# Optimization experiments

Hardware: AMD Instinct MI355X
Metric: run time of the kernel (lower is better)

## Reference

```python
import jax, jax.numpy as jnp
import numpy as np

S = 4      # num_residual_streams
V = 1      # num_input_views
ITERS = 20 # sinkhorn iters
B = 2      # batch
N = 4096   # seq len
D = 2048   # dim (num_fracs=1 so dim_eff == dim)


def setup_inputs() -> dict:
    key = jax.random.key(0)
    ks = jax.random.split(key, 6)
    return dict(
        residuals=jax.random.normal(ks[0], (B * S, N, D), jnp.float32),
        gamma=0.1 * jax.random.normal(ks[1], (S * D,), jnp.float32),
        dyn_alpha_fn=0.02 * jax.random.normal(ks[2], (S * D, S * (S + V)), jnp.float32),
        static_alpha=jax.random.normal(ks[3], (S, S + V), jnp.float32),
        pre_branch_scale=0.01 * jnp.ones((1,), jnp.float32),
        residual_scale=0.01 * jnp.ones((1,), jnp.float32),
        dyn_beta_fn=0.02 * jax.random.normal(ks[4], (S * D, S), jnp.float32),
        static_beta=jax.random.normal(ks[5], (S,), jnp.float32),
        h_post_scale=jnp.float32(0.01),
    )


def _sinkhorn(log_a, iters):
    # alternating row/col normalization in log space over last two axes
    def body(_, la):
        la = la - jax.scipy.special.logsumexp(la, axis=-2, keepdims=True)
        return la - jax.scipy.special.logsumexp(la, axis=-1, keepdims=True)
    return jnp.exp(jax.lax.fori_loop(0, iters, body, log_a))


def reference(residuals, gamma, dyn_alpha_fn, static_alpha, pre_branch_scale,
              residual_scale, dyn_beta_fn, static_beta, h_post_scale):
    bs, n, d = residuals.shape
    b = bs // S
    # '(b s) n d -> b n s d'
    r = residuals.reshape(b, S, n, d).transpose(0, 2, 1, 3)  # [b,n,S,d]
    flat = r.reshape(b, n, S * d)
    # RMSNorm: F.normalize(x, dim=-1) * sqrt(S*d) * (gamma + 1)
    nrm = flat / jnp.maximum(jnp.linalg.norm(flat, axis=-1, keepdims=True), 1e-12)
    normed = nrm * jnp.sqrt(jnp.float32(S * d)) * (gamma + 1.0)  # [b,n,S*d]

    wc = (normed @ dyn_alpha_fn).reshape(b, n, S, S + V)  # dynamic gate weights
    alpha_scale = jnp.concatenate([
        jnp.broadcast_to(pre_branch_scale, (V,)),
        jnp.broadcast_to(residual_scale, (S,)),
    ])  # [S+V]
    alpha = wc * alpha_scale + static_alpha  # [b,n,S,S+V]
    alpha_pre = jax.nn.sigmoid(alpha[..., :V])            # [b,n,S,V]
    alpha_res = _sinkhorn(alpha[..., V:], ITERS)          # doubly-stochastic [b,n,S,S]
    alpha_full = jnp.concatenate([alpha_pre, alpha_res], axis=-1)  # [b,n,S,1+S]

    # mix streams: '... s t, ... s d -> ... t d'
    mix = jnp.einsum('bnst,bnsd->bntd', alpha_full, r)  # [b,n,1+S,d]
    branch_input = mix[..., 0, :]       # [b,n,d]
    res_mix = mix[..., 1:, :]           # [b,n,S,d]

    beta = jax.nn.sigmoid((normed @ dyn_beta_fn) * h_post_scale + static_beta) * 2.0  # [b,n,S]

    # branch = identity -> branch_output == branch_input
    # depth connection: 'b n d, b n s -> b n s d', then add residual streams
    out = branch_input[..., None, :] * beta[..., :, None] + res_mix  # [b,n,S,d]
    # 'b n s d -> (b s) n d'
    return out.transpose(0, 2, 1, 3).reshape(b * S, n, d)
```

## Files before the change

### kernel.cpp

```cpp
#include <hip/hip_runtime.h>
#include <hip/hip_bf16.h>

typedef float f32x4 __attribute__((ext_vector_type(4)));
typedef float f32x16 __attribute__((ext_vector_type(16)));
typedef unsigned int u32;
typedef u32 u32x2 __attribute__((ext_vector_type(2)));
typedef u32 u32x4 __attribute__((ext_vector_type(4)));
typedef short bf16x8 __attribute__((ext_vector_type(8)));

#define SD 8192
#define NROWS 8192
#define NN 4096
#define DD 2048
#define DTP 4104

__device__ __forceinline__ u32 bfr(float f) {
    u32 u = __float_as_uint(f);
    return (u + 0x7fffu + ((u >> 16) & 1u)) >> 16;
}
__device__ __forceinline__ float blo(u32 u) { return __uint_as_float(u << 16); }
__device__ __forceinline__ float bhi(u32 u) { return __uint_as_float(u & 0xffff0000u); }

__global__ void k0_prep(const float* __restrict__ gamma,
                        const float* __restrict__ daf,
                        const float* __restrict__ dbf,
                        unsigned short* __restrict__ Wfrag) {
    int idx = blockIdx.x * 256 + threadIdx.x;
    if (idx >= 32 * SD) return;
    const int e    = idx & 7;
    const int lane = (idx >> 3) & 63;
    const int st   = (idx >> 9) & 63;
    const int wv   = idx >> 15;
    const int outk = lane & 31;
    const int j    = wv * 1024 + st * 16 + ((lane >> 5) & 1) * 8 + e;
    unsigned short v = 0;
    if (outk < 24) {
        float g = gamma[j] + 1.0f;
        float w = (outk < 20) ? daf[j * 20 + outk] : dbf[j * 4 + (outk - 20)];
        v = (unsigned short)bfr(w * g);
    }
    Wfrag[idx] = v;
}

__global__ __launch_bounds__(512) void kf(const float* __restrict__ res,
                                          const unsigned short* __restrict__ Wfrag,
                                          const float* __restrict__ sa,
                                          const float* __restrict__ sb,
                                          const float* __restrict__ pbs,
                                          const float* __restrict__ rsc,
                                          const float* __restrict__ hps,
                                          float* __restrict__ out) {
    __shared__ u32 dTp[4][DTP];
    __shared__ float pc[8][4][32];
    __shared__ float red[4][32];
    __shared__ float ssqw[8];
    __shared__ float coefS[4][16];

    const int tid  = threadIdx.x;
    const int wv   = tid >> 6;
    const int lane = tid & 63;
    const int row0 = blockIdx.x * 4;
    const int b    = row0 >> 12;
    const int n0   = row0 & (NN - 1);
    const int r    = tid >> 7;
    const int rem  = tid & 127;

    const float* rowbase = res + ((size_t)(b * 4) * NN + (n0 + r)) * DD;
    f32x4 ssq4 = {0.f, 0.f, 0.f, 0.f};
#pragma unroll 1
    for (int h = 0; h < 4; ++h) {
        f32x4 v[4];
#pragma unroll
        for (int i = 0; i < 4; ++i) {
            const int q  = h * 4 + i;
            const int j0 = (rem + 128 * q) * 4;
            const int s  = j0 >> 11, d = j0 & 2047;
            v[i] = __builtin_nontemporal_load((const f32x4*)(rowbase + (size_t)s * NN * DD + d));
        }
#pragma unroll
        for (int i = 0; i < 4; ++i) {
            ssq4 += v[i] * v[i];
            u32 lo, hi;
            asm("v_cvt_pk_bf16_f32 %0, %1, %2" : "=v"(lo) : "v"(v[i].x), "v"(v[i].y));
            asm("v_cvt_pk_bf16_f32 %0, %1, %2" : "=v"(hi) : "v"(v[i].z), "v"(v[i].w));
            const int jp = (rem + 128 * (h * 4 + i)) * 2;
            *(u32x2*)&dTp[r][jp] = (u32x2){lo, hi};
        }
    }
    float ssq = ssq4.x + ssq4.y + ssq4.z + ssq4.w;
    ssq += __shfl_xor(ssq, 1);  ssq += __shfl_xor(ssq, 2);
    ssq += __shfl_xor(ssq, 4);  ssq += __shfl_xor(ssq, 8);
    ssq += __shfl_xor(ssq, 16); ssq += __shfl_xor(ssq, 32);
    if (lane == 0) ssqw[wv] = ssq;
    __syncthreads();

    {
        f32x16 acc;
#pragma unroll
        for (int i = 0; i < 16; ++i) acc[i] = 0.f;
        const u32* abase = &dTp[lane & 3][wv * 512 + (lane >> 5) * 4];
        const unsigned short* wbase = Wfrag + ((size_t)wv * 64 * 64 + lane) * 8;
#pragma unroll 1
        for (int g = 0; g < 8; ++g) {
            u32x4 bu[8];
#pragma unroll
            for (int s = 0; s < 8; ++s)
                bu[s] = *(const u32x4*)(wbase + (size_t)(g * 8 + s) * 64 * 8);
#pragma unroll
            for (int s = 0; s < 8; ++s) {
                const u32x4 au = *(const u32x4*)(abase + (g * 8 + s) * 8);
                acc = __builtin_amdgcn_mfma_f32_32x32x16_bf16(
                    __builtin_bit_cast(bf16x8, au), __builtin_bit_cast(bf16x8, bu[s]), acc, 0, 0, 0);
            }
        }
        if (lane < 32) {
#pragma unroll
            for (int gg = 0; gg < 4; ++gg) pc[wv][gg][lane] = acc[gg];
        }
    }
    __syncthreads();
    if (tid < 128) {
        const int rr = tid >> 5, c = tid & 31;
        float s = 0.f;
#pragma unroll
        for (int w = 0; w < 8; ++w) s += pc[w][rr][c];
        red[rr][c] = s;
    }
    __syncthreads();

    if (wv == 0) {
        const int rr = lane >> 4, l = lane & 15, s = l >> 2, t = l & 3;
        const float ssqr  = ssqw[2 * rr] + ssqw[2 * rr + 1];
        const float scale = 90.50966799187809f / fmaxf(sqrtf(ssqr), 1e-12f);
        const float P  = red[rr][s * 5 + t + 1];
        const float P0 = red[rr][s * 5];
        const float Pb = red[rr][20 + t];
        float la = scale * P * rsc[0] + sa[s * 5 + t + 1];
        const float a0 = scale * P0 * pbs[0] + sa[s * 5];
        const float ap = 1.f / (1.f + __expf(-a0));
        const float bt = 2.f / (1.f + __expf(-(scale * Pb * hps[0] + sb[t])));
#pragma unroll
        for (int it = 0; it < 20; ++it) {
            float m = fmaxf(la, __shfl_xor(la, 4));
            m = fmaxf(m, __shfl_xor(m, 8));
            float e = __expf(la - m);
            e += __shfl_xor(e, 4);
            e += __shfl_xor(e, 8);
            la -= m + __logf(e);
            m = fmaxf(la, __shfl_xor(la, 1));
            m = fmaxf(m, __shfl_xor(m, 2));
            e = __expf(la - m);
            e += __shfl_xor(e, 1);
            e += __shfl_xor(e, 2);
            la -= m + __logf(e);
        }
        coefS[rr][t * 4 + s] = ap * bt + __expf(la);
    }
    __syncthreads();

    float cf[16];
#pragma unroll
    for (int i = 0; i < 16; ++i) cf[i] = coefS[r][i];
    float* ob = out + ((size_t)(b * 4) * NN + (n0 + r)) * DD;
#pragma unroll 1
    for (int qq = 0; qq < 4; ++qq) {
        const int dp = (rem + 128 * qq) * 2;
        f32x4 dv4[4];
#pragma unroll
        for (int s = 0; s < 4; ++s) {
            u32x2 u = *(const u32x2*)&dTp[r][s * 1024 + dp];
            dv4[s] = (f32x4){blo(u[0]), bhi(u[0]), blo(u[1]), bhi(u[1])};
        }
#pragma unroll
        for (int t = 0; t < 4; ++t) {
            f32x4 o = cf[t * 4 + 0] * dv4[0];
            o += cf[t * 4 + 1] * dv4[1];
            o += cf[t * 4 + 2] * dv4[2];
            o += cf[t * 4 + 3] * dv4[3];
            __builtin_nontemporal_store(o, (f32x4*)(ob + (size_t)t * NN * DD + dp * 2));
        }
    }
}

extern "C" void kernel_launch(void* const* d_in, const int* in_sizes, int n_in,
                              void* d_out, int out_size, void* d_ws, size_t ws_size,
                              hipStream_t stream) {
    const float* residuals = (const float*)d_in[0];
    const float* gamma     = (const float*)d_in[1];
    const float* daf       = (const float*)d_in[2];
    const float* sa        = (const float*)d_in[3];
    const float* pbs       = (const float*)d_in[4];
    const float* rsc       = (const float*)d_in[5];
    const float* dbf       = (const float*)d_in[6];
    const float* sb        = (const float*)d_in[7];
    const float* hps       = (const float*)d_in[8];
    float* out = (float*)d_out;

    unsigned short* Wfrag = (unsigned short*)d_ws;

    k0_prep<<<1024, 256, 0, stream>>>(gamma, daf, dbf, Wfrag);
    kf<<<NROWS / 4, 512, 0, stream>>>(residuals, Wfrag, sa, sb, pbs, rsc, hps, out);
}
```

Baseline: 152.2 us.

## Give each wave its own stream slice and interleave loads with MFMA

Each wave now loads a 1024-wide slice of one stream for all four rows of the block. That is exactly the bf16 slice its own MFMA segment consumes, so the MFMA work can start on a chunk while the next chunk is still loading. This removes the block-wide barrier between the load phase and the matmul phase. Per-row sums of squares become per-wave partials that are combined across the 8 waves in the gate stage. Residual loads lose the nontemporal hint, and LDS writes are now 64-lane strided per row, which may shift cache and bank behaviour.

```diff
diff --git a/kernel.cpp b/kernel.cpp
--- a/kernel.cpp
+++ b/kernel.cpp
@@ -53,7 +53,7 @@
     __shared__ u32 dTp[4][DTP];
     __shared__ float pc[8][4][32];
     __shared__ float red[4][32];
-    __shared__ float ssqw[8];
+    __shared__ float ssqp[8][4];
     __shared__ float coefS[4][16];
 
     const int tid  = threadIdx.x;
@@ -65,53 +65,84 @@
     const int r    = tid >> 7;
     const int rem  = tid & 127;
 
-    const float* rowbase = res + ((size_t)(b * 4) * NN + (n0 + r)) * DD;
-    f32x4 ssq4 = {0.f, 0.f, 0.f, 0.f};
-#pragma unroll 1
-    for (int h = 0; h < 4; ++h) {
-        f32x4 v[4];
-#pragma unroll
-        for (int i = 0; i < 4; ++i) {
-            const int q  = h * 4 + i;
-            const int j0 = (rem + 128 * q) * 4;
-            const int s  = j0 >> 11, d = j0 & 2047;
-            v[i] = __builtin_nontemporal_load((const f32x4*)(rowbase + (size_t)s * NN * DD + d));
-        }
-#pragma unroll
-        for (int i = 0; i < 4; ++i) {
-            ssq4 += v[i] * v[i];
-            u32 lo, hi;
-            asm("v_cvt_pk_bf16_f32 %0, %1, %2" : "=v"(lo) : "v"(v[i].x), "v"(v[i].y));
-            asm("v_cvt_pk_bf16_f32 %0, %1, %2" : "=v"(hi) : "v"(v[i].z), "v"(v[i].w));
-            const int jp = (rem + 128 * (h * 4 + i)) * 2;
-            *(u32x2*)&dTp[r][jp] = (u32x2){lo, hi};
-        }
-    }
-    float ssq = ssq4.x + ssq4.y + ssq4.z + ssq4.w;
-    ssq += __shfl_xor(ssq, 1);  ssq += __shfl_xor(ssq, 2);
-    ssq += __shfl_xor(ssq, 4);  ssq += __shfl_xor(ssq, 8);
-    ssq += __shfl_xor(ssq, 16); ssq += __shfl_xor(ssq, 32);
-    if (lane == 0) ssqw[wv] = ssq;
-    __syncthreads();
-
     {
+        const int sp = wv >> 1;
+        const int d0 = (wv & 1) * 1024;
+        const float* rp0 = res + ((size_t)(b * 4 + sp) * NN + n0) * DD + d0 + lane * 4;
+        const float* rp1 = rp0 + DD;
+        const float* rp2 = rp0 + 2 * DD;
+        const float* rp3 = rp0 + 3 * DD;
+
         f32x16 acc;
 #pragma unroll
         for (int i = 0; i < 16; ++i) acc[i] = 0.f;
+        float sq0 = 0.f, sq1 = 0.f, sq2 = 0.f, sq3 = 0.f;
         const u32* abase = &dTp[lane & 3][wv * 512 + (lane >> 5) * 4];
-        const unsigned short* wbase = Wfrag + ((size_t)wv * 64 * 64 + lane) * 8;
-#pragma unroll 1
-        for (int g = 0; g < 8; ++g) {
-            u32x4 bu[8];
-#pragma unroll
-            for (int s = 0; s < 8; ++s)
-                bu[s] = *(const u32x4*)(wbase + (size_t)(g * 8 + s) * 64 * 8);
-#pragma unroll
-            for (int s = 0; s < 8; ++s) {
-                const u32x4 au = *(const u32x4*)(abase + (g * 8 + s) * 8);
-                acc = __builtin_amdgcn_mfma_f32_32x32x16_bf16(
-                    __builtin_bit_cast(bf16x8, au), __builtin_bit_cast(bf16x8, bu[s]), acc, 0, 0, 0);
-            }
+        const unsigned short* wbase = Wfrag + ((size_t)wv * 4096 + lane) * 8;
+
+        f32x4 v0, v1, v2, v3;
+#define SG_LOAD(i)                                                            \
+        do {                                                                  \
+            v0 = *(const f32x4*)(rp0 + (i) * 256);                            \
+            v1 = *(const f32x4*)(rp1 + (i) * 256);                            \
+            v2 = *(const f32x4*)(rp2 + (i) * 256);                            \
+            v3 = *(const f32x4*)(rp3 + (i) * 256);                            \
+        } while (0)
+#define SG_FIN(i)                                                             \
+        do {                                                                  \
+            sq0 += v0.x * v0.x + v0.y * v0.y + v0.z * v0.z + v0.w * v0.w;     \
+            sq1 += v1.x * v1.x + v1.y * v1.y + v1.z * v1.z + v1.w * v1.w;     \
+            sq2 += v2.x * v2.x + v2.y * v2.y + v2.z * v2.z + v2.w * v2.w;     \
+            sq3 += v3.x * v3.x + v3.y * v3.y + v3.z * v3.z + v3.w * v3.w;     \
+            const int o = wv * 512 + (i) * 128 + lane * 2;                    \
+            u32 lo, hi;                                                       \
+            asm("v_cvt_pk_bf16_f32 %0, %1, %2" : "=v"(lo) : "v"(v0.x), "v"(v0.y)); \
+            asm("v_cvt_pk_bf16_f32 %0, %1, %2" : "=v"(hi) : "v"(v0.z), "v"(v0.w)); \
+            *(u32x2*)&dTp[0][o] = (u32x2){lo, hi};                            \
+            asm("v_cvt_pk_bf16_f32 %0, %1, %2" : "=v"(lo) : "v"(v1.x), "v"(v1.y)); \
+            asm("v_cvt_pk_bf16_f32 %0, %1, %2" : "=v"(hi) : "v"(v1.z), "v"(v1.w)); \
+            *(u32x2*)&dTp[1][o] = (u32x2){lo, hi};                            \
+            asm("v_cvt_pk_bf16_f32 %0, %1, %2" : "=v"(lo) : "v"(v2.x), "v"(v2.y)); \
+            asm("v_cvt_pk_bf16_f32 %0, %1, %2" : "=v"(hi) : "v"(v2.z), "v"(v2.w)); \
+            *(u32x2*)&dTp[2][o] = (u32x2){lo, hi};                            \
+            asm("v_cvt_pk_bf16_f32 %0, %1, %2" : "=v"(lo) : "v"(v3.x), "v"(v3.y)); \
+            asm("v_cvt_pk_bf16_f32 %0, %1, %2" : "=v"(hi) : "v"(v3.z), "v"(v3.w)); \
+            *(u32x2*)&dTp[3][o] = (u32x2){lo, hi};                            \
+        } while (0)
+#define MM(seg)                                                               \
+        do {                                                                  \
+            _Pragma("unroll")                                                 \
+            for (int g = 0; g < 2; ++g) {                                     \
+                u32x4 bu[8];                                                  \
+                _Pragma("unroll")                                             \
+                for (int s8 = 0; s8 < 8; ++s8)                                \
+                    bu[s8] = *(const u32x4*)(wbase + (size_t)((seg) * 16 + g * 8 + s8) * 512); \
+                _Pragma("unroll")                                             \
+                for (int s8 = 0; s8 < 8; ++s8) {                              \
+                    const u32x4 au = *(const u32x4*)(abase + ((seg) * 16 + g * 8 + s8) * 8); \
+                    acc = __builtin_amdgcn_mfma_f32_32x32x16_bf16(            \
+                        __builtin_bit_cast(bf16x8, au),                       \
+                        __builtin_bit_cast(bf16x8, bu[s8]), acc, 0, 0, 0);    \
+                }                                                             \
+            }                                                                 \
+        } while (0)
+
+        SG_LOAD(0); SG_FIN(0);
+        SG_LOAD(1); MM(0); SG_FIN(1);
+        SG_LOAD(2); MM(1); SG_FIN(2);
+        SG_LOAD(3); MM(2); SG_FIN(3);
+        MM(3);
+#undef SG_LOAD
+#undef SG_FIN
+#undef MM
+
+#define RED64(x) x += __shfl_xor(x, 1); x += __shfl_xor(x, 2); x += __shfl_xor(x, 4); \
+                 x += __shfl_xor(x, 8); x += __shfl_xor(x, 16); x += __shfl_xor(x, 32);
+        RED64(sq0) RED64(sq1) RED64(sq2) RED64(sq3)
+#undef RED64
+        if (lane == 0) {
+            ssqp[wv][0] = sq0; ssqp[wv][1] = sq1;
+            ssqp[wv][2] = sq2; ssqp[wv][3] = sq3;
         }
         if (lane < 32) {
 #pragma unroll
@@ -130,7 +161,9 @@
 
     if (wv == 0) {
         const int rr = lane >> 4, l = lane & 15, s = l >> 2, t = l & 3;
-        const float ssqr  = ssqw[2 * rr] + ssqw[2 * rr + 1];
+        float ssqr = 0.f;
+#pragma unroll
+        for (int w = 0; w < 8; ++w) ssqr += ssqp[w][rr];
         const float scale = 90.50966799187809f / fmaxf(sqrtf(ssqr), 1e-12f);
         const float P  = red[rr][s * 5 + t + 1];
         const float P0 = red[rr][s * 5];
```

Measured after the change: 176.2 us. 15.8% more time.

## Split fused kernel into coefficient pass and streaming mix pass rereading residuals

Applied to the files above, without the earlier changes.

Replaces the single fused kernel, which staged all four streams as bf16 in shared memory, with two kernels. The first streams residuals directly into MFMA fragments with register double-buffering to compute the norms, gates and Sinkhorn coefficients, and writes them to workspace. The second rereads fp32 residuals in reverse row order to exploit cache, then mixes and writes the output. This removes the large LDS footprint that limited occupancy, at the cost of reading the residuals a second time.

```diff
diff --git a/kernel.cpp b/kernel.cpp
--- a/kernel.cpp
+++ b/kernel.cpp
@@ -4,7 +4,6 @@
 typedef float f32x4 __attribute__((ext_vector_type(4)));
 typedef float f32x16 __attribute__((ext_vector_type(16)));
 typedef unsigned int u32;
-typedef u32 u32x2 __attribute__((ext_vector_type(2)));
 typedef u32 u32x4 __attribute__((ext_vector_type(4)));
 typedef short bf16x8 __attribute__((ext_vector_type(8)));
 
@@ -12,7 +11,7 @@
 #define NROWS 8192
 #define NN 4096
 #define DD 2048
-#define DTP 4104
+#define PLANE ((size_t)NN * DD)
 
 __device__ __forceinline__ u32 bfr(float f) {
     u32 u = __float_as_uint(f);
@@ -29,10 +28,9 @@
     if (idx >= 32 * SD) return;
     const int e    = idx & 7;
     const int lane = (idx >> 3) & 63;
-    const int st   = (idx >> 9) & 63;
-    const int wv   = idx >> 15;
+    const int stg  = idx >> 9;
     const int outk = lane & 31;
-    const int j    = wv * 1024 + st * 16 + ((lane >> 5) & 1) * 8 + e;
+    const int j    = stg * 16 + ((lane >> 5) & 1) * 8 + e;
     unsigned short v = 0;
     if (outk < 24) {
         float g = gamma[j] + 1.0f;
@@ -42,99 +40,104 @@
     Wfrag[idx] = v;
 }
 
-__global__ __launch_bounds__(512) void kf(const float* __restrict__ res,
-                                          const unsigned short* __restrict__ Wfrag,
-                                          const float* __restrict__ sa,
-                                          const float* __restrict__ sb,
-                                          const float* __restrict__ pbs,
-                                          const float* __restrict__ rsc,
-                                          const float* __restrict__ hps,
-                                          float* __restrict__ out) {
-    __shared__ u32 dTp[4][DTP];
-    __shared__ float pc[8][4][32];
-    __shared__ float red[4][32];
-    __shared__ float ssqw[8];
-    __shared__ float coefS[4][16];
+__global__ __launch_bounds__(256) void k1p(const float* __restrict__ res,
+                                           const unsigned short* __restrict__ Wfrag,
+                                           const float* __restrict__ sa,
+                                           const float* __restrict__ sb,
+                                           const float* __restrict__ pbs,
+                                           const float* __restrict__ rsc,
+                                           const float* __restrict__ hps,
+                                           float* __restrict__ Coef) {
+    __shared__ float pc[4][4][32];
+    __shared__ float ssqp[4][4];
 
     const int tid  = threadIdx.x;
     const int wv   = tid >> 6;
     const int lane = tid & 63;
-    const int row0 = blockIdx.x * 4;
+    const int row0 = blockIdx.x * 8;
     const int b    = row0 >> 12;
     const int n0   = row0 & (NN - 1);
-    const int r    = tid >> 7;
-    const int rem  = tid & 127;
-
-    const float* rowbase = res + ((size_t)(b * 4) * NN + (n0 + r)) * DD;
-    f32x4 ssq4 = {0.f, 0.f, 0.f, 0.f};
+    const int rg   = wv >> 1, h = wv & 1;
+    const int dr   = lane & 3, hi = lane >> 5;
+
+    const float* p0 = res + ((size_t)(b * 4 + h * 2) * NN + (n0 + rg * 4 + dr)) * DD + hi * 8;
+    const unsigned short* wb = Wfrag + ((size_t)(h * 256) * 64 + lane) * 8;
+
+    f32x16 acc;
+#pragma unroll
+    for (int i = 0; i < 16; ++i) acc[i] = 0.f;
+    f32x4 sq4 = {0.f, 0.f, 0.f, 0.f};
+    f32x4 aA[8], aB[8];
+
+#define LDA(BUF, G)                                                           \
+    do {                                                                      \
+        const int st0_ = (G) * 4;                                             \
+        const float* pp_ = p0 + ((st0_ & 128) ? PLANE : 0) + (size_t)(st0_ & 127) * 16; \
+        BUF[0] = *(const f32x4*)(pp_);      BUF[1] = *(const f32x4*)(pp_ + 4);  \
+        BUF[2] = *(const f32x4*)(pp_ + 16); BUF[3] = *(const f32x4*)(pp_ + 20); \
+        BUF[4] = *(const f32x4*)(pp_ + 32); BUF[5] = *(const f32x4*)(pp_ + 36); \
+        BUF[6] = *(const f32x4*)(pp_ + 48); BUF[7] = *(const f32x4*)(pp_ + 52); \
+    } while (0)
+
+#define CMP(BUF, BU)                                                          \
+    do {                                                                      \
+        _Pragma("unroll")                                                     \
+        for (int k_ = 0; k_ < 4; ++k_) {                                      \
+            const f32x4 v0_ = BUF[2 * k_], v1_ = BUF[2 * k_ + 1];             \
+            sq4 += v0_ * v0_;                                                 \
+            sq4 += v1_ * v1_;                                                 \
+            u32 c0_, c1_, c2_, c3_;                                           \
+            asm("v_cvt_pk_bf16_f32 %0, %1, %2" : "=v"(c0_) : "v"(v0_.x), "v"(v0_.y)); \
+            asm("v_cvt_pk_bf16_f32 %0, %1, %2" : "=v"(c1_) : "v"(v0_.z), "v"(v0_.w)); \
+            asm("v_cvt_pk_bf16_f32 %0, %1, %2" : "=v"(c2_) : "v"(v1_.x), "v"(v1_.y)); \
+            asm("v_cvt_pk_bf16_f32 %0, %1, %2" : "=v"(c3_) : "v"(v1_.z), "v"(v1_.w)); \
+            const u32x4 au_ = {c0_, c1_, c2_, c3_};                           \
+            acc = __builtin_amdgcn_mfma_f32_32x32x16_bf16(                    \
+                __builtin_bit_cast(bf16x8, au_),                              \
+                __builtin_bit_cast(bf16x8, BU[k_]), acc, 0, 0, 0);            \
+        }                                                                     \
+    } while (0)
+
+    LDA(aA, 0);
 #pragma unroll 1
-    for (int h = 0; h < 4; ++h) {
-        f32x4 v[4];
-#pragma unroll
-        for (int i = 0; i < 4; ++i) {
-            const int q  = h * 4 + i;
-            const int j0 = (rem + 128 * q) * 4;
-            const int s  = j0 >> 11, d = j0 & 2047;
-            v[i] = __builtin_nontemporal_load((const f32x4*)(rowbase + (size_t)s * NN * DD + d));
-        }
-#pragma unroll
-        for (int i = 0; i < 4; ++i) {
-            ssq4 += v[i] * v[i];
-            u32 lo, hi;
-            asm("v_cvt_pk_bf16_f32 %0, %1, %2" : "=v"(lo) : "v"(v[i].x), "v"(v[i].y));
-            asm("v_cvt_pk_bf16_f32 %0, %1, %2" : "=v"(hi) : "v"(v[i].z), "v"(v[i].w));
-            const int jp = (rem + 128 * (h * 4 + i)) * 2;
-            *(u32x2*)&dTp[r][jp] = (u32x2){lo, hi};
-        }
-    }
-    float ssq = ssq4.x + ssq4.y + ssq4.z + ssq4.w;
-    ssq += __shfl_xor(ssq, 1);  ssq += __shfl_xor(ssq, 2);
+    for (int gp = 0; gp < 32; ++gp) {
+        const int g0 = gp * 2, g1 = g0 + 1;
+        u32x4 bu0[4];
+#pragma unroll
+        for (int k = 0; k < 4; ++k)
+            bu0[k] = *(const u32x4*)(wb + (size_t)(g0 * 4 + k) * 512);
+        LDA(aB, g1);
+        CMP(aA, bu0);
+        u32x4 bu1[4];
+#pragma unroll
+        for (int k = 0; k < 4; ++k)
+            bu1[k] = *(const u32x4*)(wb + (size_t)(g1 * 4 + k) * 512);
+        const int gn = (gp < 31) ? g1 + 1 : 63;
+        LDA(aA, gn);
+        CMP(aB, bu1);
+    }
+#undef LDA
+#undef CMP
+
+    float ssq = sq4.x + sq4.y + sq4.z + sq4.w;
     ssq += __shfl_xor(ssq, 4);  ssq += __shfl_xor(ssq, 8);
     ssq += __shfl_xor(ssq, 16); ssq += __shfl_xor(ssq, 32);
-    if (lane == 0) ssqw[wv] = ssq;
+    if (lane < 4) ssqp[wv][lane] = ssq;
+    if (lane < 32) {
+#pragma unroll
+        for (int gg = 0; gg < 4; ++gg) pc[wv][gg][lane] = acc[gg];
+    }
     __syncthreads();
 
-    {
-        f32x16 acc;
-#pragma unroll
-        for (int i = 0; i < 16; ++i) acc[i] = 0.f;
-        const u32* abase = &dTp[lane & 3][wv * 512 + (lane >> 5) * 4];
-        const unsigned short* wbase = Wfrag + ((size_t)wv * 64 * 64 + lane) * 8;
-#pragma unroll 1
-        for (int g = 0; g < 8; ++g) {
-            u32x4 bu[8];
-#pragma unroll
-            for (int s = 0; s < 8; ++s)
-                bu[s] = *(const u32x4*)(wbase + (size_t)(g * 8 + s) * 64 * 8);
-#pragma unroll
-            for (int s = 0; s < 8; ++s) {
-                const u32x4 au = *(const u32x4*)(abase + (g * 8 + s) * 8);
-                acc = __builtin_amdgcn_mfma_f32_32x32x16_bf16(
-                    __builtin_bit_cast(bf16x8, au), __builtin_bit_cast(bf16x8, bu[s]), acc, 0, 0, 0);
-            }
-        }
-        if (lane < 32) {
-#pragma unroll
-            for (int gg = 0; gg < 4; ++gg) pc[wv][gg][lane] = acc[gg];
-        }
-    }
-    __syncthreads();
     if (tid < 128) {
-        const int rr = tid >> 5, c = tid & 31;
-        float s = 0.f;
-#pragma unroll
-        for (int w = 0; w < 8; ++w) s += pc[w][rr][c];
-        red[rr][c] = s;
-    }
-    __syncthreads();
-
-    if (wv == 0) {
-        const int rr = lane >> 4, l = lane & 15, s = l >> 2, t = l & 3;
-        const float ssqr  = ssqw[2 * rr] + ssqw[2 * rr + 1];
+        const int rr = tid >> 4;
+        const int l = tid & 15, s = l >> 2, t = l & 3;
+        const int w0 = (rr >> 2) * 2, w1 = w0 + 1, r4 = rr & 3;
+        const float ssqr = (ssqp[w0][r4] + ssqp[w1][r4]) * 0.125f;
         const float scale = 90.50966799187809f / fmaxf(sqrtf(ssqr), 1e-12f);
-        const float P  = red[rr][s * 5 + t + 1];
-        const float P0 = red[rr][s * 5];
-        const float Pb = red[rr][20 + t];
+        const float P  = pc[w0][r4][s * 5 + t + 1] + pc[w1][r4][s * 5 + t + 1];
+        const float P0 = pc[w0][r4][s * 5]         + pc[w1][r4][s * 5];
+        const float Pb = pc[w0][r4][20 + t]        + pc[w1][r4][20 + t];
         float la = scale * P * rsc[0] + sa[s * 5 + t + 1];
         const float a0 = scale * P0 * pbs[0] + sa[s * 5];
         const float ap = 1.f / (1.f + __expf(-a0));
@@ -154,32 +157,38 @@
             e += __shfl_xor(e, 2);
             la -= m + __logf(e);
         }
-        coefS[rr][t * 4 + s] = ap * bt + __expf(la);
-    }
-    __syncthreads();
-
+        Coef[(size_t)(row0 + rr) * 16 + t * 4 + s] = ap * bt + __expf(la);
+    }
+}
+
+__global__ __launch_bounds__(256) void k3_mix(const float* __restrict__ res,
+                                              const float* __restrict__ Coef,
+                                              float* __restrict__ out) {
+    const int row = (NROWS - 1) - blockIdx.x;
+    const int b = row >> 12, n = row & (NN - 1);
+    const int tid = threadIdx.x;
     float cf[16];
 #pragma unroll
-    for (int i = 0; i < 16; ++i) cf[i] = coefS[r][i];
-    float* ob = out + ((size_t)(b * 4) * NN + (n0 + r)) * DD;
-#pragma unroll 1
-    for (int qq = 0; qq < 4; ++qq) {
-        const int dp = (rem + 128 * qq) * 2;
-        f32x4 dv4[4];
-#pragma unroll
-        for (int s = 0; s < 4; ++s) {
-            u32x2 u = *(const u32x2*)&dTp[r][s * 1024 + dp];
-            dv4[s] = (f32x4){blo(u[0]), bhi(u[0]), blo(u[1]), bhi(u[1])};
+    for (int i = 0; i < 16; ++i) cf[i] = Coef[(size_t)row * 16 + i];
+    f32x4 rv[4][2];
+#pragma unroll
+    for (int s = 0; s < 4; ++s)
+#pragma unroll
+        for (int p = 0; p < 2; ++p) {
+            const size_t g = ((size_t)(b * 4 + s) * NN + n) * DD + p * 1024 + tid * 4;
+            rv[s][p] = *(const f32x4*)(res + g);
         }
 #pragma unroll
-        for (int t = 0; t < 4; ++t) {
-            f32x4 o = cf[t * 4 + 0] * dv4[0];
-            o += cf[t * 4 + 1] * dv4[1];
-            o += cf[t * 4 + 2] * dv4[2];
-            o += cf[t * 4 + 3] * dv4[3];
-            __builtin_nontemporal_store(o, (f32x4*)(ob + (size_t)t * NN * DD + dp * 2));
+    for (int t = 0; t < 4; ++t)
+#pragma unroll
+        for (int p = 0; p < 2; ++p) {
+            f32x4 o = cf[t * 4 + 0] * rv[0][p];
+            o += cf[t * 4 + 1] * rv[1][p];
+            o += cf[t * 4 + 2] * rv[2][p];
+            o += cf[t * 4 + 3] * rv[3][p];
+            const size_t g = ((size_t)(b * 4 + t) * NN + n) * DD + p * 1024 + tid * 4;
+            __builtin_nontemporal_store(o, (f32x4*)(out + g));
         }
-    }
 }
 
 extern "C" void kernel_launch(void* const* d_in, const int* in_sizes, int n_in,
@@ -197,7 +206,9 @@
     float* out = (float*)d_out;
 
     unsigned short* Wfrag = (unsigned short*)d_ws;
+    float* Coef = (float*)((char*)d_ws + (1 << 19));
 
     k0_prep<<<1024, 256, 0, stream>>>(gamma, daf, dbf, Wfrag);
-    kf<<<NROWS / 4, 512, 0, stream>>>(residuals, Wfrag, sa, sb, pbs, rsc, hps, out);
-}
+    k1p<<<1024, 256, 0, stream>>>(residuals, Wfrag, sa, sb, pbs, rsc, hps, Coef);
+    k3_mix<<<NROWS, 256, 0, stream>>>(residuals, Coef, out);
+}
```

Result: slower. 348.7 us (+129.2%).

## Software-pipeline residual loads with MFMA projection in chunked loop

Applied to the files above, without the earlier changes.

Restructures the fused kernel so each row's residual data is loaded in eight chunks. Each chunk is converted to bf16 in LDS and immediately consumed by MFMA, while the next chunk's global loads are already in flight. Per-chunk block barriers replace the single load-all-then-compute phase, and the weight fragment layout changes so each chunk maps to the matching K slice. It also drops nontemporal hints on the loads. The aim is to overlap HBM reads with the projection matmul, at the cost of eight barriers per block and possible ordering hazards on LDS reuse.

```diff
diff --git a/kernel.cpp b/kernel.cpp
--- a/kernel.cpp
+++ b/kernel.cpp
@@ -29,10 +29,9 @@
     if (idx >= 32 * SD) return;
     const int e    = idx & 7;
     const int lane = (idx >> 3) & 63;
-    const int st   = (idx >> 9) & 63;
-    const int wv   = idx >> 15;
+    const int stg  = idx >> 9;
     const int outk = lane & 31;
-    const int j    = wv * 1024 + st * 16 + ((lane >> 5) & 1) * 8 + e;
+    const int j    = stg * 16 + ((lane >> 5) & 1) * 8 + e;
     unsigned short v = 0;
     if (outk < 24) {
         float g = gamma[j] + 1.0f;
@@ -65,54 +64,64 @@
     const int r    = tid >> 7;
     const int rem  = tid & 127;
 
-    const float* rowbase = res + ((size_t)(b * 4) * NN + (n0 + r)) * DD;
-    f32x4 ssq4 = {0.f, 0.f, 0.f, 0.f};
+    {
+        const float* rowbase = res + ((size_t)(b * 4) * NN + (n0 + r)) * DD;
+        const u32* abase = &dTp[lane & 3][wv * 64 + (lane >> 5) * 4];
+        const unsigned short* wb0 = Wfrag + (size_t)lane * 8;
+
+        f32x16 acc;
+#pragma unroll
+        for (int i = 0; i < 16; ++i) acc[i] = 0.f;
+        float ssq = 0.f;
+
+        f32x4 v0, v1;
+        {
+            const int j0 = rem * 8;
+            const int s = j0 >> 11, d = j0 & 2047;
+            const float* p = rowbase + (size_t)s * NN * DD + d;
+            v0 = *(const f32x4*)(p);
+            v1 = *(const f32x4*)(p + 4);
+        }
 #pragma unroll 1
-    for (int h = 0; h < 4; ++h) {
-        f32x4 v[4];
-#pragma unroll
-        for (int i = 0; i < 4; ++i) {
-            const int q  = h * 4 + i;
-            const int j0 = (rem + 128 * q) * 4;
-            const int s  = j0 >> 11, d = j0 & 2047;
-            v[i] = __builtin_nontemporal_load((const f32x4*)(rowbase + (size_t)s * NN * DD + d));
-        }
-#pragma unroll
-        for (int i = 0; i < 4; ++i) {
-            ssq4 += v[i] * v[i];
-            u32 lo, hi;
-            asm("v_cvt_pk_bf16_f32 %0, %1, %2" : "=v"(lo) : "v"(v[i].x), "v"(v[i].y));
-            asm("v_cvt_pk_bf16_f32 %0, %1, %2" : "=v"(hi) : "v"(v[i].z), "v"(v[i].w));
-            const int jp = (rem + 128 * (h * 4 + i)) * 2;
-            *(u32x2*)&dTp[r][jp] = (u32x2){lo, hi};
-        }
-    }
-    float ssq = ssq4.x + ssq4.y + ssq4.z + ssq4.w;
-    ssq += __shfl_xor(ssq, 1);  ssq += __shfl_xor(ssq, 2);
-    ssq += __shfl_xor(ssq, 4);  ssq += __shfl_xor(ssq, 8);
-    ssq += __shfl_xor(ssq, 16); ssq += __shfl_xor(ssq, 32);
-    if (lane == 0) ssqw[wv] = ssq;
-    __syncthreads();
-
-    {
-        f32x16 acc;
-#pragma unroll
-        for (int i = 0; i < 16; ++i) acc[i] = 0.f;
-        const u32* abase = &dTp[lane & 3][wv * 512 + (lane >> 5) * 4];
-        const unsigned short* wbase = Wfrag + ((size_t)wv * 64 * 64 + lane) * 8;
-#pragma unroll 1
-        for (int g = 0; g < 8; ++g) {
+        for (int t = 0; t < 8; ++t) {
+            ssq += v0.x * v0.x + v0.y * v0.y + v0.z * v0.z + v0.w * v0.w;
+            ssq += v1.x * v1.x + v1.y * v1.y + v1.z * v1.z + v1.w * v1.w;
+            {
+                u32 c0, c1, c2, c3;
+                asm("v_cvt_pk_bf16_f32 %0, %1, %2" : "=v"(c0) : "v"(v0.x), "v"(v0.y));
+                asm("v_cvt_pk_bf16_f32 %0, %1, %2" : "=v"(c1) : "v"(v0.z), "v"(v0.w));
+                asm("v_cvt_pk_bf16_f32 %0, %1, %2" : "=v"(c2) : "v"(v1.x), "v"(v1.y));
+                asm("v_cvt_pk_bf16_f32 %0, %1, %2" : "=v"(c3) : "v"(v1.z), "v"(v1.w));
+                *(u32x4*)&dTp[r][t * 512 + rem * 4] = (u32x4){c0, c1, c2, c3};
+            }
             u32x4 bu[8];
 #pragma unroll
-            for (int s = 0; s < 8; ++s)
-                bu[s] = *(const u32x4*)(wbase + (size_t)(g * 8 + s) * 64 * 8);
-#pragma unroll
-            for (int s = 0; s < 8; ++s) {
-                const u32x4 au = *(const u32x4*)(abase + (g * 8 + s) * 8);
+            for (int s8 = 0; s8 < 8; ++s8)
+                bu[s8] = *(const u32x4*)(wb0 + (size_t)((t * 64 + wv * 8 + s8) * 64) * 8);
+            if (t < 7) {
+                const int j0 = (t + 1) * 1024 + rem * 8;
+                const int s = j0 >> 11, d = j0 & 2047;
+                const float* p = rowbase + (size_t)s * NN * DD + d;
+                v0 = *(const f32x4*)(p);
+                v1 = *(const f32x4*)(p + 4);
+            }
+            asm volatile("s_waitcnt lgkmcnt(0)" ::: "memory");
+            __builtin_amdgcn_sched_barrier(0);
+            __builtin_amdgcn_s_barrier();
+#pragma unroll
+            for (int s8 = 0; s8 < 8; ++s8) {
+                const u32x4 au = *(const u32x4*)(abase + t * 512 + s8 * 8);
                 acc = __builtin_amdgcn_mfma_f32_32x32x16_bf16(
-                    __builtin_bit_cast(bf16x8, au), __builtin_bit_cast(bf16x8, bu[s]), acc, 0, 0, 0);
+                    __builtin_bit_cast(bf16x8, au),
+                    __builtin_bit_cast(bf16x8, bu[s8]), acc, 0, 0, 0);
             }
-        }
+            __builtin_amdgcn_sched_barrier(0);
+        }
+
+        ssq += __shfl_xor(ssq, 1);  ssq += __shfl_xor(ssq, 2);
+        ssq += __shfl_xor(ssq, 4);  ssq += __shfl_xor(ssq, 8);
+        ssq += __shfl_xor(ssq, 16); ssq += __shfl_xor(ssq, 32);
+        if (lane == 0) ssqw[wv] = ssq;
         if (lane < 32) {
 #pragma unroll
             for (int gg = 0; gg < 4; ++gg) pc[wv][gg][lane] = acc[gg];
```

Measured after the change: 125.3 us. -17.7%, faster.
